# Kernel tuning notes

Hardware: AMD Instinct MI355X
Metric: run time of the kernel (lower is better)

The kernel has to match this reference:

```python
import jax, jax.numpy as jnp
import numpy as np

B, T, HID = 2, 2048, 2048
H, D, K = 16, 128, 4
EPS = 1e-6


def _short_conv(x, w):
    # depthwise causal conv1d + SiLU; x: [B,T,C], w: [C,K]
    Tlen = x.shape[1]
    xp = jnp.pad(x, ((0, 0), (K - 1, 0), (0, 0)))
    y = sum(xp[:, j:j + Tlen, :] * w[:, j] for j in range(K))
    return y * jax.nn.sigmoid(y)


def _l2norm(x):
    return x * jax.lax.rsqrt(jnp.sum(x * x, axis=-1, keepdims=True) + EPS)


def setup_inputs() -> dict:
    key = jax.random.key(0)
    ks = jax.random.split(key, 16)
    nrm = lambda k, shape, s=0.02: jax.random.normal(k, shape, jnp.float32) * s
    return {
        "hidden_states": jax.random.normal(ks[0], (B, T, HID), jnp.float32),
        "Wq": nrm(ks[1], (HID, H * D)),
        "Wk": nrm(ks[2], (HID, H * D)),
        "Wv": nrm(ks[3], (HID, H * D)),
        "conv_wq": nrm(ks[4], (H * D, K), 0.3),
        "conv_wk": nrm(ks[5], (H * D, K), 0.3),
        "conv_wv": nrm(ks[6], (H * D, K), 0.3),
        "A_log": jnp.log(jax.random.uniform(ks[7], (H,), jnp.float32, 1.0, 16.0)),
        "dt_bias": nrm(ks[8], (H * D,), 0.5),
        "Wfa": nrm(ks[9], (HID, D)),
        "Wfb": nrm(ks[10], (D, H * D)),
        "Wb": nrm(ks[11], (HID, H)),
        "Wga": nrm(ks[12], (HID, D)),
        "Wgb": nrm(ks[13], (D, H * D)),
        "norm_w": jnp.ones((D,), jnp.float32),
        "Wo": nrm(ks[14], (H * D, HID)),
    }


def reference(hidden_states, Wq, Wk, Wv, conv_wq, conv_wk, conv_wv, A_log,
              dt_bias, Wfa, Wfb, Wb, Wga, Wgb, norm_w, Wo):
    h = hidden_states  # [B,T,HID]
    q = _short_conv(h @ Wq, conv_wq).reshape(B, T, H, D)
    k = _short_conv(h @ Wk, conv_wk).reshape(B, T, H, D)
    v = _short_conv(h @ Wv, conv_wv).reshape(B, T, H, D)

    # fused_kda_gate: g = -exp(A_log) * softplus(f(x) + dt_bias), per-channel log-decay
    g = ((h @ Wfa) @ Wfb).reshape(B, T, H, D)
    g = -jnp.exp(A_log)[None, None, :, None] * jax.nn.softplus(g + dt_bias.reshape(H, D))

    beta = jax.nn.sigmoid(h @ Wb)  # [B,T,H]

    q = _l2norm(q) * (D ** -0.5)
    k = _l2norm(k)

    # gated delta-rule recurrence over time; state S: [B,H,Dk,Dv]
    def step(S, inp):
        q_t, k_t, v_t, g_t, b_t = inp
        S = S * jnp.exp(g_t)[..., None]                      # per-key-channel decay
        kS = jnp.einsum('bhk,bhkv->bhv', k_t, S)             # k^T S
        delta = b_t[..., None] * (v_t - kS)                  # delta-rule correction
        S = S + jnp.einsum('bhk,bhv->bhkv', k_t, delta)
        o_t = jnp.einsum('bhk,bhkv->bhv', q_t, S)
        return S, o_t

    S0 = jnp.zeros((B, H, D, D), jnp.float32)
    xs = (q.transpose(1, 0, 2, 3), k.transpose(1, 0, 2, 3),
          v.transpose(1, 0, 2, 3), g.transpose(1, 0, 2, 3),
          beta.transpose(1, 0, 2))
    _, o = jax.lax.scan(step, S0, xs)
    o = o.transpose(1, 0, 2, 3)  # [B,T,H,D]

    # gated RMSNorm over head_dim with sigmoid gate
    gate = ((h @ Wga) @ Wgb).reshape(B, T, H, D)
    o = o * jax.lax.rsqrt(jnp.mean(o * o, axis=-1, keepdims=True) + EPS) * norm_w
    o = o * jax.nn.sigmoid(gate)

    return o.reshape(B * T, H * D) @ Wo  # [(B*T), HID]
```

## Files before the change

### kernel.cpp

```cpp
#include <hip/hip_runtime.h>
#include <hip/hip_bf16.h>


using short8 = __attribute__((ext_vector_type(8))) short;
using f32x4  = __attribute__((ext_vector_type(4))) float;

static __device__ __forceinline__ ushort f2bf(float f) {
    __hip_bfloat16 h = __float2bfloat16(f);
    return *reinterpret_cast<ushort*>(&h);
}

static __device__ __forceinline__ float qadd1(float x) {
    int y = __builtin_amdgcn_mov_dpp(__float_as_int(x), 0xB1, 0xF, 0xF, true);
    return x + __int_as_float(y);
}
static __device__ __forceinline__ float qadd2(float x) {
    int y = __builtin_amdgcn_mov_dpp(__float_as_int(x), 0x4E, 0xF, 0xF, true);
    return x + __int_as_float(y);
}
static __device__ __forceinline__ float radd4(float x) {
    int y = __builtin_amdgcn_mov_dpp(__float_as_int(x), 0x124, 0xF, 0xF, true);
    return x + __int_as_float(y);
}
static __device__ __forceinline__ float radd8(float x) {
    int y = __builtin_amdgcn_mov_dpp(__float_as_int(x), 0x128, 0xF, 0xF, true);
    return x + __int_as_float(y);
}
static __device__ __forceinline__ float rsum16(float x) {
    x = qadd1(x);
    x = qadd2(x);
    x = radd4(x);
    x = radd8(x);
    return x;
}

template<int W, int R> struct BufIdx { static constexpr int w = W, r = R; };

__global__ __launch_bounds__(256) void cast_bf16(const float* __restrict__ in,
                                                 ushort* __restrict__ out, int n8)
{
    const int i = blockIdx.x * 256 + threadIdx.x;
    if (i >= n8) return;
    const float4 a = ((const float4*)in)[2 * i];
    const float4 b = ((const float4*)in)[2 * i + 1];
    ushort u[8] = {f2bf(a.x), f2bf(a.y), f2bf(a.z), f2bf(a.w),
                   f2bf(b.x), f2bf(b.y), f2bf(b.z), f2bf(b.w)};
    ((uint4*)out)[i] = *(uint4*)u;
}

__global__ __launch_bounds__(256) void tcast(const float* __restrict__ in,
                                             ushort* __restrict__ out,
                                             int R, int C)
{
    __shared__ float tile[64][68];
    const int t  = threadIdx.x;
    const int c0 = blockIdx.x * 64, r0 = blockIdx.y * 64;
    const int lr = t >> 2, lc = (t & 3) * 16;
#pragma unroll
    for (int j = 0; j < 4; ++j) {
        const float4 v = *(const float4*)&in[(size_t)(r0 + lr) * C + c0 + lc + 4 * j];
        *(float4*)&tile[lr][lc + 4 * j] = v;
    }
    __syncthreads();
    const int oc = t >> 2, och = (t & 3) * 16;
    uint u[8];
#pragma unroll
    for (int j = 0; j < 8; ++j) {
        const float f0 = tile[och + 2 * j][oc];
        const float f1 = tile[och + 2 * j + 1][oc];
        u[j] = (uint)f2bf(f0) | ((uint)f2bf(f1) << 16);
    }
    uint4* dst = (uint4*)&out[(size_t)(c0 + oc) * R + r0 + och];
    dst[0] = make_uint4(u[0], u[1], u[2], u[3]);
    dst[1] = make_uint4(u[4], u[5], u[6], u[7]);
}

template<bool OUT16>
__global__ __launch_bounds__(256) void gemm_bf16(
    const ushort* __restrict__ A0, const ushort* __restrict__ A1,
    const ushort* __restrict__ A2, const ushort* __restrict__ A3,
    const ushort* __restrict__ B0, const ushort* __restrict__ B1,
    const ushort* __restrict__ B2, const ushort* __restrict__ B3,
    void* __restrict__ C0, void* __restrict__ C1,
    void* __restrict__ C2, void* __restrict__ C3,
    int M, int N, int K)
{
    const int z = blockIdx.z;
    const ushort* A = (z == 0) ? A0 : (z == 1) ? A1 : (z == 2) ? A2 : A3;
    const ushort* B = (z == 0) ? B0 : (z == 1) ? B1 : (z == 2) ? B2 : B3;
    void* Cv       = (z == 0) ? C0 : (z == 1) ? C1 : (z == 2) ? C2 : C3;

    __shared__ ushort As[128 * 64];
    __shared__ ushort Bs[128 * 64];

    const int tid  = threadIdx.x;
    const int lane = tid & 63;
    const int wave = tid >> 6;
    const int wm = wave >> 1, wn = wave & 1;
    const int bm = blockIdx.x * 128, bn = blockIdx.y * 128;

    const int srow  = tid >> 1;
    const int spart = tid & 1;

    const int ml = lane & 15;
    const int g  = lane >> 4;

    f32x4 acc[4][4];
#pragma unroll
    for (int i = 0; i < 4; ++i)
#pragma unroll
        for (int j = 0; j < 4; ++j) acc[i][j] = (f32x4){0.f, 0.f, 0.f, 0.f};

    const size_t arow_off = (size_t)(bm + srow) * K;
    const size_t brow_off = (size_t)(bn + srow) * K;

    for (int k0 = 0; k0 < K; k0 += 64) {
#pragma unroll
        for (int j = 0; j < 4; ++j) {
            const int ch = spart * 4 + j;
            const int sw = ((srow * 128 + ch * 16) ^ ((srow & 7) << 4)) >> 1;
            *(uint4*)&As[sw] = *(const uint4*)&A[arow_off + k0 + ch * 8];
            *(uint4*)&Bs[sw] = *(const uint4*)&B[brow_off + k0 + ch * 8];
        }
        __syncthreads();
#pragma unroll
        for (int kk = 0; kk < 2; ++kk) {
            short8 af[4], bfr[4];
#pragma unroll
            for (int mi = 0; mi < 4; ++mi) {
                const int row = wm * 64 + mi * 16 + ml;
                const int sw  = ((row * 128 + (kk * 4 + g) * 16) ^ ((ml & 7) << 4)) >> 1;
                af[mi] = *(const short8*)&As[sw];
            }
#pragma unroll
            for (int ni = 0; ni < 4; ++ni) {
                const int row = wn * 64 + ni * 16 + ml;
                const int sw  = ((row * 128 + (kk * 4 + g) * 16) ^ ((ml & 7) << 4)) >> 1;
                bfr[ni] = *(const short8*)&Bs[sw];
            }
#pragma unroll
            for (int mi = 0; mi < 4; ++mi)
#pragma unroll
                for (int ni = 0; ni < 4; ++ni)
                    acc[mi][ni] = __builtin_amdgcn_mfma_f32_16x16x32_bf16(
                        af[mi], bfr[ni], acc[mi][ni], 0, 0, 0);
        }
        __syncthreads();
    }

#pragma unroll
    for (int mi = 0; mi < 4; ++mi)
#pragma unroll
        for (int ni = 0; ni < 4; ++ni) {
            const int col = bn + wn * 64 + ni * 16 + ml;
#pragma unroll
            for (int r = 0; r < 4; ++r) {
                const int row = bm + wm * 64 + mi * 16 + g * 4 + r;
                if constexpr (OUT16) {
                    ((ushort*)Cv)[(size_t)row * N + col] = f2bf(acc[mi][ni][r]);
                } else {
                    ((float*)Cv)[(size_t)row * N + col] = acc[mi][ni][r];
                }
            }
        }
}

__global__ __launch_bounds__(256) void gemm_n16(
    const float* __restrict__ A, const float* __restrict__ B,
    float* __restrict__ C, int M, int Kd)
{
    const int tid  = threadIdx.x;
    const int n    = tid & 15;
    const int mloc = tid >> 4;
    const int m    = blockIdx.x * 16 + mloc;
    const float* a  = A + (size_t)m * Kd;
    const float* bn = B + n;
    float acc = 0.f;
#pragma unroll 4
    for (int k0 = 0; k0 < Kd; k0 += 8) {
        float4 a0 = *(const float4*)(a + k0);
        float4 a1 = *(const float4*)(a + k0 + 4);
        acc = fmaf(a0.x, bn[(size_t)(k0 + 0) * 16], acc);
        acc = fmaf(a0.y, bn[(size_t)(k0 + 1) * 16], acc);
        acc = fmaf(a0.z, bn[(size_t)(k0 + 2) * 16], acc);
        acc = fmaf(a0.w, bn[(size_t)(k0 + 3) * 16], acc);
        acc = fmaf(a1.x, bn[(size_t)(k0 + 4) * 16], acc);
        acc = fmaf(a1.y, bn[(size_t)(k0 + 5) * 16], acc);
        acc = fmaf(a1.z, bn[(size_t)(k0 + 6) * 16], acc);
        acc = fmaf(a1.w, bn[(size_t)(k0 + 7) * 16], acc);
    }
    C[(size_t)m * 16 + n] = acc;
}

__global__ __launch_bounds__(256) void halo_save(
    const float* __restrict__ q, const float* __restrict__ k,
    const float* __restrict__ v, float* __restrict__ hal)
{
    constexpr int T = 2048, C = 2048, SEG = 512;
    const int idx = blockIdx.x * 256 + threadIdx.x;
    const int cid = idx % 12288;
    const int sh  = idx / 12288;
    const int sg  = sh / 3 + 1;
    const int ho  = sh % 3;
    const int which = cid >> 12, rem = cid & 4095, b = rem >> 11, c = rem & 2047;
    const float* x = (which == 0) ? q : (which == 1) ? k : v;
    hal[idx] = x[(size_t)b * T * C + (size_t)(sg * SEG - 3 + ho) * C + c];
}

__global__ __launch_bounds__(256) void conv_silu(
    float* __restrict__ q, float* __restrict__ k, float* __restrict__ v,
    const float* __restrict__ wq, const float* __restrict__ wk,
    const float* __restrict__ wv, const float* __restrict__ hal)
{
    constexpr int T = 2048, C = 2048, SEG = 512;
    const int seg    = blockIdx.x & 3;
    const int colblk = blockIdx.x >> 2;
    const int cid    = colblk * 256 + threadIdx.x;
    const int which  = cid >> 12;
    const int rem    = cid & 4095;
    const int b      = rem >> 11;
    const int c      = rem & 2047;
    float* x        = (which == 0) ? q : (which == 1) ? k : v;
    const float* w  = (which == 0) ? wq : (which == 1) ? wk : wv;

    const float w0 = w[c * 4 + 0], w1 = w[c * 4 + 1];
    const float w2 = w[c * 4 + 2], w3 = w[c * 4 + 3];
    float* p = x + (size_t)b * T * C + c;
    float xm3, xm2, xm1;
    if (seg == 0) { xm3 = xm2 = xm1 = 0.f; }
    else {
        xm3 = hal[((seg - 1) * 3 + 0) * 12288 + cid];
        xm2 = hal[((seg - 1) * 3 + 1) * 12288 + cid];
        xm1 = hal[((seg - 1) * 3 + 2) * 12288 + cid];
    }

    const int t0s = seg * SEG;
    for (int t0 = t0s; t0 < t0s + SEG; t0 += 16) {
        float xt[16], yo[16];
#pragma unroll
        for (int j = 0; j < 16; ++j) xt[j] = p[(size_t)(t0 + j) * C];
#pragma unroll
        for (int j = 0; j < 16; ++j) {
            float y = fmaf(xm3, w0, fmaf(xm2, w1, fmaf(xm1, w2, xt[j] * w3)));
            yo[j] = y / (1.f + __expf(-y));
            xm3 = xm2; xm2 = xm1; xm1 = xt[j];
        }
#pragma unroll
        for (int j = 0; j < 16; ++j) p[(size_t)(t0 + j) * C] = yo[j];
    }
}

__global__ __launch_bounds__(256) void prep_qkg(
    float* __restrict__ Qb, float* __restrict__ Kb, float* __restrict__ Gb,
    const float* __restrict__ A_log, const float* __restrict__ dt_bias,
    int rows)
{
    const int wave = threadIdx.x >> 6;
    const int lane = threadIdx.x & 63;
    const int row  = blockIdx.x * 4 + wave;
    if (row >= rows) return;
    const int hh = row & 15;
    const size_t base = (size_t)row * 128;

    float q0 = Qb[base + lane], q1 = Qb[base + 64 + lane];
    float k0 = Kb[base + lane], k1 = Kb[base + 64 + lane];
    float sq = q0 * q0 + q1 * q1;
    float sk = k0 * k0 + k1 * k1;
#pragma unroll
    for (int off = 32; off >= 1; off >>= 1) {
        sq += __shfl_xor(sq, off);
        sk += __shfl_xor(sk, off);
    }
    const float qs = rsqrtf(sq + 1e-6f) * 0.08838834764831845f;
    const float ks = rsqrtf(sk + 1e-6f);
    Qb[base + lane] = q0 * qs; Qb[base + 64 + lane] = q1 * qs;
    Kb[base + lane] = k0 * ks; Kb[base + 64 + lane] = k1 * ks;

    const float a = __expf(A_log[hh]);
    float x0 = Gb[base + lane]      + dt_bias[hh * 128 + lane];
    float x1 = Gb[base + 64 + lane] + dt_bias[hh * 128 + 64 + lane];
    float sp0 = (x0 > 20.f) ? x0 : log1pf(__expf(x0));
    float sp1 = (x1 > 20.f) ? x1 : log1pf(__expf(x1));
    Gb[base + lane]      = __expf(-a * sp0);
    Gb[base + 64 + lane] = __expf(-a * sp1);
}

__global__ __launch_bounds__(64, 1) void kda_scan(
    const float* __restrict__ Q, const float* __restrict__ Kk,
    const float* __restrict__ V, const float* __restrict__ EG,
    const float* __restrict__ Braw, float* __restrict__ O)
{
    constexpr int T = 2048, H = 16, HD = 2048;
    const int bid = blockIdx.x;
    const int bh  = bid & 31;
    const int vg  = bid >> 5;
    const int b = bh >> 4, hh = bh & 15;
    const int lane = threadIdx.x;
    const int col  = lane >> 4;
    const int sl   = lane & 15;
    const int vcol = vg * 4 + col;

    __shared__ __align__(16) float k_s[3][128];
    __shared__ __align__(16) float e_s[3][128];
    __shared__ __align__(16) float q_s[3][128];

    float s[8];
#pragma unroll
    for (int i = 0; i < 8; ++i) s[i] = 0.f;

    const size_t tok0 = (size_t)b * T;
    const int cb = hh * 128;
    const float* qp = Q  + tok0 * HD + cb;
    const float* kp = Kk + tok0 * HD + cb;
    const float* ep = EG + tok0 * HD + cb;
    const float* vp = V  + tok0 * HD + cb;
    const float* bp = Braw + tok0 * H + hh;
    float* op = O + tok0 * HD + cb;

    const int d0 = 2 * lane;
    const int cw = lane >> 1;
    const int pw = cw ^ (cw >> 3);
    const int stpos = pw * 4 + (d0 & 3);

    const int c0r = 2 * sl, c1r = 2 * sl + 1;
    const int rof0 = (c0r ^ (c0r >> 3)) << 2;
    const int rof1 = (c1r ^ (c1r >> 3)) << 2;

    {
        *(float2*)&k_s[0][stpos] = *(const float2*)&kp[d0];
        *(float2*)&e_s[0][stpos] = *(const float2*)&ep[d0];
        *(float2*)&q_s[0][stpos] = *(const float2*)&qp[d0];
        *(float2*)&k_s[1][stpos] = *(const float2*)&kp[HD + d0];
        *(float2*)&e_s[1][stpos] = *(const float2*)&ep[HD + d0];
        *(float2*)&q_s[1][stpos] = *(const float2*)&qp[HD + d0];
    }
    float2 FaK = *(const float2*)&kp[(size_t)2 * HD + d0];
    float2 FaE = *(const float2*)&ep[(size_t)2 * HD + d0];
    float2 FaQ = *(const float2*)&qp[(size_t)2 * HD + d0];
    float2 FbK = *(const float2*)&kp[(size_t)3 * HD + d0];
    float2 FbE = *(const float2*)&ep[(size_t)3 * HD + d0];
    float2 FbQ = *(const float2*)&qp[(size_t)3 * HD + d0];
    float v0 = vp[vcol];
    float v1 = vp[(size_t)1 * HD + vcol];
    float v2 = vp[(size_t)2 * HD + vcol];
    float v3 = vp[(size_t)3 * HD + vcol];
    float beta = 1.f / (1.f + __expf(-bp[0]));
    float br1 = bp[(size_t)1 * H];
    float br2 = bp[(size_t)2 * H];
    float br3 = bp[(size_t)3 * H];

    __syncthreads();

    float4 KX[2], EX[2], QX[2], KY[2], EY[2], QY[2];
    KX[0] = *(const float4*)&k_s[0][rof0];
    KX[1] = *(const float4*)&k_s[0][rof1];
    EX[0] = *(const float4*)&e_s[0][rof0];
    EX[1] = *(const float4*)&e_s[0][rof1];
    QX[0] = *(const float4*)&q_s[0][rof0];
    QX[1] = *(const float4*)&q_s[0][rof1];

    auto step = [&](auto bi, const int t,
                    float4* KF, float4* EF, float4* QF,
                    float4* KG, float4* EGr, float4* QG,
                    float2& Fk, float2& Fe, float2& Fq) {
        constexpr int W = decltype(bi)::w;
        constexpr int R = decltype(bi)::r;
        KG[0]  = *(const float4*)&k_s[R][rof0];
        KG[1]  = *(const float4*)&k_s[R][rof1];
        EGr[0] = *(const float4*)&e_s[R][rof0];
        EGr[1] = *(const float4*)&e_s[R][rof1];
        QG[0]  = *(const float4*)&q_s[R][rof0];
        QG[1]  = *(const float4*)&q_s[R][rof1];
        *(float2*)&k_s[W][stpos] = Fk;
        *(float2*)&e_s[W][stpos] = Fe;
        *(float2*)&q_s[W][stpos] = Fq;
        {
            const size_t o4 = (size_t)(t + 4) * HD;
            Fk = *(const float2*)&kp[o4 + d0];
            Fe = *(const float2*)&ep[o4 + d0];
            Fq = *(const float2*)&qp[o4 + d0];
        }
        float a0, a1, a2, a3;
        {
            float s0 = s[0] * EF[0].x, s1 = s[1] * EF[0].y;
            float s2 = s[2] * EF[0].z, s3 = s[3] * EF[0].w;
            float s4 = s[4] * EF[1].x, s5 = s[5] * EF[1].y;
            float s6 = s[6] * EF[1].z, s7 = s[7] * EF[1].w;
            s[0] = s0; s[1] = s1; s[2] = s2; s[3] = s3;
            s[4] = s4; s[5] = s5; s[6] = s6; s[7] = s7;
            a0 = KF[0].x * s0; a1 = KF[0].y * s1;
            a2 = KF[0].z * s2; a3 = KF[0].w * s3;
            a0 = fmaf(KF[1].x, s4, a0); a1 = fmaf(KF[1].y, s5, a1);
            a2 = fmaf(KF[1].z, s6, a2); a3 = fmaf(KF[1].w, s7, a3);
        }
        float kS = rsum16((a0 + a1) + (a2 + a3));
        const float delta = beta * (v0 - kS);
        float o0, o1, o2v, o3v;
        {
            float s0 = fmaf(KF[0].x, delta, s[0]);
            float s1 = fmaf(KF[0].y, delta, s[1]);
            float s2 = fmaf(KF[0].z, delta, s[2]);
            float s3 = fmaf(KF[0].w, delta, s[3]);
            float s4 = fmaf(KF[1].x, delta, s[4]);
            float s5 = fmaf(KF[1].y, delta, s[5]);
            float s6 = fmaf(KF[1].z, delta, s[6]);
            float s7 = fmaf(KF[1].w, delta, s[7]);
            s[0] = s0; s[1] = s1; s[2] = s2; s[3] = s3;
            s[4] = s4; s[5] = s5; s[6] = s6; s[7] = s7;
            o0 = QF[0].x * s0; o1 = QF[0].y * s1;
            o2v = QF[0].z * s2; o3v = QF[0].w * s3;
            o0 = fmaf(QF[1].x, s4, o0); o1 = fmaf(QF[1].y, s5, o1);
            o2v = fmaf(QF[1].z, s6, o2v); o3v = fmaf(QF[1].w, s7, o3v);
        }
        float oo = rsum16((o0 + o1) + (o2v + o3v));
        if (sl == 0) op[(size_t)t * HD + vcol] = oo;
        {
            const float vn = vp[(size_t)(t + 4) * HD + vcol];
            const float bn = bp[(size_t)(t + 4) * H];
            v0 = v1; v1 = v2; v2 = v3; v3 = vn;
            beta = 1.f / (1.f + __expf(-br1));
            br1 = br2; br2 = br3; br3 = bn;
        }
    };

    for (int t = 0; t < T - 2; t += 6) {
        step(BufIdx<2, 1>{}, t + 0, KX, EX, QX, KY, EY, QY, FaK, FaE, FaQ);
        step(BufIdx<0, 2>{}, t + 1, KY, EY, QY, KX, EX, QX, FbK, FbE, FbQ);
        step(BufIdx<1, 0>{}, t + 2, KX, EX, QX, KY, EY, QY, FaK, FaE, FaQ);
        step(BufIdx<2, 1>{}, t + 3, KY, EY, QY, KX, EX, QX, FbK, FbE, FbQ);
        step(BufIdx<0, 2>{}, t + 4, KX, EX, QX, KY, EY, QY, FaK, FaE, FaQ);
        step(BufIdx<1, 0>{}, t + 5, KY, EY, QY, KX, EX, QX, FbK, FbE, FbQ);
    }
    step(BufIdx<2, 1>{}, T - 2, KX, EX, QX, KY, EY, QY, FaK, FaE, FaQ);
    step(BufIdx<0, 2>{}, T - 1, KY, EY, QY, KX, EX, QX, FbK, FbE, FbQ);
}

__global__ __launch_bounds__(256) void norm_gate(
    const float* __restrict__ O, const float* __restrict__ Gate,
    const float* __restrict__ norm_w, ushort* __restrict__ Out16, int rows)
{
    const int wave = threadIdx.x >> 6;
    const int lane = threadIdx.x & 63;
    const int row  = blockIdx.x * 4 + wave;
    if (row >= rows) return;
    const size_t base = (size_t)row * 128;

    float o0 = O[base + lane], o1 = O[base + 64 + lane];
    float ss = o0 * o0 + o1 * o1;
#pragma unroll
    for (int off = 32; off >= 1; off >>= 1) ss += __shfl_xor(ss, off);
    const float scale = rsqrtf(ss * (1.f / 128.f) + 1e-6f);

    const float g0 = Gate[base + lane], g1 = Gate[base + 64 + lane];
    o0 = o0 * scale * norm_w[lane]      * (1.f / (1.f + __expf(-g0)));
    o1 = o1 * scale * norm_w[64 + lane] * (1.f / (1.f + __expf(-g1)));
    Out16[base + lane]      = f2bf(o0);
    Out16[base + 64 + lane] = f2bf(o1);
}

extern "C" void kernel_launch(void* const* d_in, const int* in_sizes, int n_in,
                              void* d_out, int out_size, void* d_ws, size_t ws_size,
                              hipStream_t stream)
{
    const float* h    = (const float*)d_in[0];
    const float* Wq   = (const float*)d_in[1];
    const float* Wk   = (const float*)d_in[2];
    const float* Wv   = (const float*)d_in[3];
    const float* cwq  = (const float*)d_in[4];
    const float* cwk  = (const float*)d_in[5];
    const float* cwv  = (const float*)d_in[6];
    const float* A_log= (const float*)d_in[7];
    const float* dtb  = (const float*)d_in[8];
    const float* Wfa  = (const float*)d_in[9];
    const float* Wfb  = (const float*)d_in[10];
    const float* Wb   = (const float*)d_in[11];
    const float* Wga  = (const float*)d_in[12];
    const float* Wgb  = (const float*)d_in[13];
    const float* nw   = (const float*)d_in[14];
    const float* Wo   = (const float*)d_in[15];
    float* out = (float*)d_out;

    const int M = 4096, HID = 2048;
    const size_t big = (size_t)M * HID;
    float* ws    = (float*)d_ws;
    float* qb    = ws;
    float* kb    = qb + big;
    float* vb    = kb + big;
    float* gb    = vb + big;
    float* ob    = gb + big;
    float* betab = ob + big;
    float* halb  = betab + (size_t)M * 16;
    ushort* hb16 = (ushort*)(halb + 110592);
    ushort* wqT  = hb16 + big;
    ushort* wkT  = wqT + (size_t)HID * HID;
    ushort* wvT  = wkT + (size_t)HID * HID;
    ushort* wfT  = wvT + (size_t)HID * HID;
    ushort* tfbT = wfT + (size_t)HID * HID;
    ushort* wfa16= tfbT + (size_t)HID * 128;

    float*  gateb = qb;
    ushort* obb16 = (ushort*)vb;

    dim3 blk(256);

    cast_bf16<<<dim3(4096), blk, 0, stream>>>(h, hb16, (int)(big / 8));
    tcast<<<dim3(32, 32), blk, 0, stream>>>(Wq, wqT, HID, HID);
    tcast<<<dim3(32, 32), blk, 0, stream>>>(Wk, wkT, HID, HID);
    tcast<<<dim3(32, 32), blk, 0, stream>>>(Wv, wvT, HID, HID);

    tcast<<<dim3(32, 2), blk, 0, stream>>>(Wfb, tfbT, 128, HID);
    cast_bf16<<<dim3(128), blk, 0, stream>>>(Wfa, wfa16, (int)((size_t)HID * 128 / 8));
    gemm_bf16<true><<<dim3(16, 16, 1), blk, 0, stream>>>(
        tfbT, tfbT, tfbT, tfbT, wfa16, wfa16, wfa16, wfa16,
        wfT, wfT, wfT, wfT, HID, HID, 128);

    gemm_bf16<false><<<dim3(32, 16, 4), blk, 0, stream>>>(
        hb16, hb16, hb16, hb16, wqT, wkT, wvT, wfT,
        qb, kb, vb, gb, M, HID, HID);

    gemm_n16<<<dim3(M / 16), blk, 0, stream>>>(h, Wb, betab, M, HID);

    halo_save<<<dim3(432), blk, 0, stream>>>(qb, kb, vb, halb);
    conv_silu<<<dim3(192), blk, 0, stream>>>(qb, kb, vb, cwq, cwk, cwv, halb);

    prep_qkg<<<dim3(16384), blk, 0, stream>>>(qb, kb, gb, A_log, dtb, M * 16);

    kda_scan<<<dim3(1024), dim3(64), 0, stream>>>(qb, kb, vb, gb, betab, ob);

    tcast<<<dim3(32, 2), blk, 0, stream>>>(Wgb, tfbT, 128, HID);
    cast_bf16<<<dim3(128), blk, 0, stream>>>(Wga, wfa16, (int)((size_t)HID * 128 / 8));
    gemm_bf16<true><<<dim3(16, 16, 1), blk, 0, stream>>>(
        tfbT, tfbT, tfbT, tfbT, wfa16, wfa16, wfa16, wfa16,
        wqT, wqT, wqT, wqT, HID, HID, 128);
    gemm_bf16<false><<<dim3(32, 16, 1), blk, 0, stream>>>(
        hb16, hb16, hb16, hb16, wqT, wqT, wqT, wqT,
        gateb, gateb, gateb, gateb, M, HID, HID);

    norm_gate<<<dim3(16384), blk, 0, stream>>>(ob, gateb, nw, obb16, M * 16);

    tcast<<<dim3(32, 32), blk, 0, stream>>>(Wo, wkT, HID, HID);
    gemm_bf16<false><<<dim3(32, 16, 1), blk, 0, stream>>>(
        obb16, obb16, obb16, obb16, wkT, wkT, wkT, wkT,
        out, out, out, out, M, HID, HID);
}
```

Baseline: 1.242 ms.

## Split scan key dimension across two half-waves, doubling scan blocks

Each scan wavefront now handles 2 value columns instead of 4, with each column's 128 key rows spread over 32 lanes holding 4 state values each instead of 16 lanes holding 8. The cross-half reduction uses a permlane32 swap after the 16-lane DPP sum. The grid doubles to 2048 blocks and launch bounds allow 2 blocks per CU. The aim is to shorten the per-step dependent chain and raise parallelism in the latency-bound recurrence. The cost is one extra cross-lane step per reduction and twice as many redundant loads of k, q and g across blocks.

```diff
diff --git a/kernel.cpp b/kernel.cpp
--- a/kernel.cpp
+++ b/kernel.cpp
@@ -4,6 +4,7 @@
 
 using short8 = __attribute__((ext_vector_type(8))) short;
 using f32x4  = __attribute__((ext_vector_type(4))) float;
+using uint2v = __attribute__((ext_vector_type(2))) unsigned int;
 
 static __device__ __forceinline__ ushort f2bf(float f) {
     __hip_bfloat16 h = __float2bfloat16(f);
@@ -32,6 +33,11 @@
     x = radd4(x);
     x = radd8(x);
     return x;
+}
+static __device__ __forceinline__ float crosssum32(float x) {
+    const unsigned xi = (unsigned)__float_as_int(x);
+    uint2v r = __builtin_amdgcn_permlane32_swap(xi, xi, false, false);
+    return __int_as_float((int)r.x) + __int_as_float((int)r.y);
 }
 
 template<int W, int R> struct BufIdx { static constexpr int w = W, r = R; };
@@ -285,7 +291,7 @@
     Gb[base + 64 + lane] = __expf(-a * sp1);
 }
 
-__global__ __launch_bounds__(64, 1) void kda_scan(
+__global__ __launch_bounds__(64, 2) void kda_scan(
     const float* __restrict__ Q, const float* __restrict__ Kk,
     const float* __restrict__ V, const float* __restrict__ EG,
     const float* __restrict__ Braw, float* __restrict__ O)
@@ -296,17 +302,17 @@
     const int vg  = bid >> 5;
     const int b = bh >> 4, hh = bh & 15;
     const int lane = threadIdx.x;
-    const int col  = lane >> 4;
-    const int sl   = lane & 15;
-    const int vcol = vg * 4 + col;
+    const int col  = (lane >> 4) & 1;
+    const int sl   = (lane & 15) | (((lane >> 5) & 1) << 4);
+    const int vcol = vg * 2 + col;
 
     __shared__ __align__(16) float k_s[3][128];
     __shared__ __align__(16) float e_s[3][128];
     __shared__ __align__(16) float q_s[3][128];
 
-    float s[8];
-#pragma unroll
-    for (int i = 0; i < 8; ++i) s[i] = 0.f;
+    float s[4];
+#pragma unroll
+    for (int i = 0; i < 4; ++i) s[i] = 0.f;
 
     const size_t tok0 = (size_t)b * T;
     const int cb = hh * 128;
@@ -322,9 +328,7 @@
     const int pw = cw ^ (cw >> 3);
     const int stpos = pw * 4 + (d0 & 3);
 
-    const int c0r = 2 * sl, c1r = 2 * sl + 1;
-    const int rof0 = (c0r ^ (c0r >> 3)) << 2;
-    const int rof1 = (c1r ^ (c1r >> 3)) << 2;
+    const int rof = (sl ^ (sl >> 3)) << 2;
 
     {
         *(float2*)&k_s[0][stpos] = *(const float2*)&kp[d0];
@@ -351,26 +355,20 @@
 
     __syncthreads();
 
-    float4 KX[2], EX[2], QX[2], KY[2], EY[2], QY[2];
-    KX[0] = *(const float4*)&k_s[0][rof0];
-    KX[1] = *(const float4*)&k_s[0][rof1];
-    EX[0] = *(const float4*)&e_s[0][rof0];
-    EX[1] = *(const float4*)&e_s[0][rof1];
-    QX[0] = *(const float4*)&q_s[0][rof0];
-    QX[1] = *(const float4*)&q_s[0][rof1];
+    float4 KX, EX, QX, KY, EY, QY;
+    KX = *(const float4*)&k_s[0][rof];
+    EX = *(const float4*)&e_s[0][rof];
+    QX = *(const float4*)&q_s[0][rof];
 
     auto step = [&](auto bi, const int t,
-                    float4* KF, float4* EF, float4* QF,
-                    float4* KG, float4* EGr, float4* QG,
+                    float4& KF, float4& EF, float4& QF,
+                    float4& KG, float4& EGr, float4& QG,
                     float2& Fk, float2& Fe, float2& Fq) {
         constexpr int W = decltype(bi)::w;
         constexpr int R = decltype(bi)::r;
-        KG[0]  = *(const float4*)&k_s[R][rof0];
-        KG[1]  = *(const float4*)&k_s[R][rof1];
-        EGr[0] = *(const float4*)&e_s[R][rof0];
-        EGr[1] = *(const float4*)&e_s[R][rof1];
-        QG[0]  = *(const float4*)&q_s[R][rof0];
-        QG[1]  = *(const float4*)&q_s[R][rof1];
+        KG  = *(const float4*)&k_s[R][rof];
+        EGr = *(const float4*)&e_s[R][rof];
+        QG  = *(const float4*)&q_s[R][rof];
         *(float2*)&k_s[W][stpos] = Fk;
         *(float2*)&e_s[W][stpos] = Fe;
         *(float2*)&q_s[W][stpos] = Fq;
@@ -380,39 +378,21 @@
             Fe = *(const float2*)&ep[o4 + d0];
             Fq = *(const float2*)&qp[o4 + d0];
         }
-        float a0, a1, a2, a3;
-        {
-            float s0 = s[0] * EF[0].x, s1 = s[1] * EF[0].y;
-            float s2 = s[2] * EF[0].z, s3 = s[3] * EF[0].w;
-            float s4 = s[4] * EF[1].x, s5 = s[5] * EF[1].y;
-            float s6 = s[6] * EF[1].z, s7 = s[7] * EF[1].w;
-            s[0] = s0; s[1] = s1; s[2] = s2; s[3] = s3;
-            s[4] = s4; s[5] = s5; s[6] = s6; s[7] = s7;
-            a0 = KF[0].x * s0; a1 = KF[0].y * s1;
-            a2 = KF[0].z * s2; a3 = KF[0].w * s3;
-            a0 = fmaf(KF[1].x, s4, a0); a1 = fmaf(KF[1].y, s5, a1);
-            a2 = fmaf(KF[1].z, s6, a2); a3 = fmaf(KF[1].w, s7, a3);
-        }
-        float kS = rsum16((a0 + a1) + (a2 + a3));
+        float s0 = s[0] * EF.x, s1 = s[1] * EF.y;
+        float s2 = s[2] * EF.z, s3 = s[3] * EF.w;
+        s[0] = s0; s[1] = s1; s[2] = s2; s[3] = s3;
+        float a0 = KF.x * s0, a1 = KF.y * s1;
+        float a2 = KF.z * s2, a3 = KF.w * s3;
+        float kS = crosssum32(rsum16((a0 + a1) + (a2 + a3)));
         const float delta = beta * (v0 - kS);
-        float o0, o1, o2v, o3v;
-        {
-            float s0 = fmaf(KF[0].x, delta, s[0]);
-            float s1 = fmaf(KF[0].y, delta, s[1]);
-            float s2 = fmaf(KF[0].z, delta, s[2]);
-            float s3 = fmaf(KF[0].w, delta, s[3]);
-            float s4 = fmaf(KF[1].x, delta, s[4]);
-            float s5 = fmaf(KF[1].y, delta, s[5]);
-            float s6 = fmaf(KF[1].z, delta, s[6]);
-            float s7 = fmaf(KF[1].w, delta, s[7]);
-            s[0] = s0; s[1] = s1; s[2] = s2; s[3] = s3;
-            s[4] = s4; s[5] = s5; s[6] = s6; s[7] = s7;
-            o0 = QF[0].x * s0; o1 = QF[0].y * s1;
-            o2v = QF[0].z * s2; o3v = QF[0].w * s3;
-            o0 = fmaf(QF[1].x, s4, o0); o1 = fmaf(QF[1].y, s5, o1);
-            o2v = fmaf(QF[1].z, s6, o2v); o3v = fmaf(QF[1].w, s7, o3v);
-        }
-        float oo = rsum16((o0 + o1) + (o2v + o3v));
+        float t0v = fmaf(KF.x, delta, s[0]);
+        float t1v = fmaf(KF.y, delta, s[1]);
+        float t2v = fmaf(KF.z, delta, s[2]);
+        float t3v = fmaf(KF.w, delta, s[3]);
+        s[0] = t0v; s[1] = t1v; s[2] = t2v; s[3] = t3v;
+        float o0 = QF.x * t0v, o1 = QF.y * t1v;
+        float o2v = QF.z * t2v, o3v = QF.w * t3v;
+        float oo = crosssum32(rsum16((o0 + o1) + (o2v + o3v)));
         if (sl == 0) op[(size_t)t * HD + vcol] = oo;
         {
             const float vn = vp[(size_t)(t + 4) * HD + vcol];
@@ -525,7 +505,7 @@
 
     prep_qkg<<<dim3(16384), blk, 0, stream>>>(qb, kb, gb, A_log, dtb, M * 16);
 
-    kda_scan<<<dim3(1024), dim3(64), 0, stream>>>(qb, kb, vb, gb, betab, ob);
+    kda_scan<<<dim3(2048), dim3(64), 0, stream>>>(qb, kb, vb, gb, betab, ob);
 
     tcast<<<dim3(32, 2), blk, 0, stream>>>(Wgb, tfbT, 128, HID);
     cast_bf16<<<dim3(128), blk, 0, stream>>>(Wga, wfa16, (int)((size_t)HID * 128 / 8));
```

Measured after the change: 1.311 ms. 1.06x slower.
